# Kernel optimization log

Measured on AMD Instinct MI355X. Metric: run time of the kernel, lower is better.

The kernel has to match this reference:

```python
import jax, jax.numpy as jnp
import numpy as np

# Window-batch of 16x16 windows from a U-Net stage
B, C, H, W = 128, 128, 16, 16
HEADS = 8
EQK, EV = 128, 512      # embed_dim_qk, embed_dim_v (embed_dim=512, ratio=4)
L = H * W               # tokens per window (stride=1)


def _conv3x3(x, w, b):
    # NCHW 3x3 conv, padding 1
    out = jax.lax.conv_general_dilated(x, w, (1, 1), ((1, 1), (1, 1)),
                                       dimension_numbers=('NCHW', 'OIHW', 'NCHW'))
    return out + b[None, :, None, None]


def _pos_att(q, wq, bq, wk, bk, wv, bv, wo, bo, gamma):
    # MultiHeadAttention2D_POS, stride=1 -> conv_q/k/v are 1x1 convs
    hd, hdv = EQK // HEADS, EV // HEADS

    def proj(x, w, bias, d):
        y = jnp.einsum('bchw,ec->behw', x, w) + bias[None, :, None, None]
        return y.reshape(B, HEADS, d, L).transpose(0, 1, 3, 2)  # (B,h,L,d)

    pq = proj(q, wq, bq, hd)
    pk = proj(q, wk, bk, hd)
    pv = proj(q, wv, bv, hdv)
    attn = jax.nn.softmax(jnp.einsum('bhqd,bhkd->bhqk', pq, pk) * hd ** -0.5, axis=-1)
    out = jnp.einsum('bhqk,bhkd->bhqd', attn, pv)
    out = out.transpose(0, 1, 3, 2).reshape(B, EV, H, W)
    out = _conv3x3(out, wo, bo)             # proj_out: 3x3 conv EV->C
    return q + out * gamma                  # gamma-scaled residual


def _cha_att(q, wq, bq, wk, bk, wv, bv, wo, bo, gamma):
    # MultiHeadAttention2D_CHA: depthwise 1x1 grouped convs (channel multiplier = HEADS),
    # attention over the CHANNEL axis. Faithfully reproduces torch's reshape of the
    # group-major (c*HEADS+h) channel layout into (B, heads, C, L).
    def dwproj(x, w, bias):
        y = (x[:, :, None] * w.reshape(C, HEADS)[None, :, :, None, None]
             + bias.reshape(C, HEADS)[None, :, :, None, None])
        return y.reshape(B, C * HEADS, H, W).reshape(B, HEADS, C, L)

    pq = dwproj(q, wq, bq)
    pk = dwproj(q, wk, bk)
    pv = dwproj(q, wv, bv)
    attn = jax.nn.softmax(jnp.einsum('bhcl,bhdl->bhcd', pq, pk) * L ** -0.5, axis=-1)
    out = jnp.einsum('bhcd,bhdl->bhcl', attn, pv)      # (B,h,C,L)
    out = out.reshape(B, HEADS * C, H, W)
    # proj_out: grouped 1x1 ConvTranspose (== grouped 1x1 conv): sum each HEADS-sized group
    out = (out.reshape(B, C, HEADS, H, W)
           * wo.reshape(C, HEADS)[None, :, :, None, None]).sum(2) + bo[None, :, None, None]
    return q + out * gamma


def _forward(qkv_pos, qkv_cha,
             pos_wq, pos_bq, pos_wk, pos_bk, pos_wv, pos_bv, pos_wo, pos_bo, gamma_pos,
             cha_wq, cha_bq, cha_wk, cha_bk, cha_wv, cha_bv, cha_wo, cha_bo, gamma_cha,
             fuse_w, fuse_b):
    out_pos = _pos_att(qkv_pos, pos_wq, pos_bq, pos_wk, pos_bk, pos_wv, pos_bv,
                       pos_wo, pos_bo, gamma_pos)
    out_cha = _cha_att(qkv_cha, cha_wq, cha_bq, cha_wk, cha_bk, cha_wv, cha_bv,
                       cha_wo, cha_bo, gamma_cha)
    out = (out_pos + out_cha) * 0.5          # att_fusion='add' (slides=0 -> full slices)
    return _conv3x3(out, fuse_w, fuse_b)     # conv_out (Dropout2d is identity at eval)


def setup_inputs() -> dict:
    key = jax.random.key(0)
    ks = jax.random.split(key, 24)
    n = lambda k, shape, s=0.05: jax.random.normal(k, shape, dtype=jnp.float32) * s
    return {
        'qkv_pos': jax.random.normal(ks[0], (B, C, H, W), jnp.float32),
        'qkv_cha': jax.random.normal(ks[1], (B, C, H, W), jnp.float32),
        'pos_wq': n(ks[2], (EQK, C)), 'pos_bq': n(ks[3], (EQK,)),
        'pos_wk': n(ks[4], (EQK, C)), 'pos_bk': n(ks[5], (EQK,)),
        'pos_wv': n(ks[6], (EV, C)), 'pos_bv': n(ks[7], (EV,)),
        'pos_wo': n(ks[8], (C, EV, 3, 3)), 'pos_bo': n(ks[9], (C,)),
        'gamma_pos': jnp.array(0.1, jnp.float32),
        'cha_wq': n(ks[10], (C * HEADS,)), 'cha_bq': n(ks[11], (C * HEADS,)),
        'cha_wk': n(ks[12], (C * HEADS,)), 'cha_bk': n(ks[13], (C * HEADS,)),
        'cha_wv': n(ks[14], (C * HEADS,)), 'cha_bv': n(ks[15], (C * HEADS,)),
        'cha_wo': n(ks[16], (C * HEADS,)), 'cha_bo': n(ks[17], (C,)),
        'gamma_cha': jnp.array(0.1, jnp.float32),
        'fuse_w': n(ks[18], (C, C, 3, 3)), 'fuse_b': n(ks[19], (C,)),
    }


def reference(qkv_pos, qkv_cha,
              pos_wq, pos_bq, pos_wk, pos_bk, pos_wv, pos_bv, pos_wo, pos_bo, gamma_pos,
              cha_wq, cha_bq, cha_wk, cha_bk, cha_wv, cha_bv, cha_wo, cha_bo, gamma_cha,
              fuse_w, fuse_b):
    return _forward(qkv_pos, qkv_cha,
                    pos_wq, pos_bq, pos_wk, pos_bk, pos_wv, pos_bv, pos_wo, pos_bo, gamma_pos,
                    cha_wq, cha_bq, cha_wk, cha_bk, cha_wv, cha_bv, cha_wo, cha_bo, gamma_cha,
                    fuse_w, fuse_b)
```

## Files before the change

kernel.cpp:

```cpp
#include <hip/hip_runtime.h>
#include <cstdint>
#include <cstddef>

typedef unsigned short ushort_t;
typedef unsigned int uint_t;
typedef __attribute__((ext_vector_type(8))) short bf16x8;
typedef __attribute__((ext_vector_type(4))) float f32x4;

#define NB 128
#define NC 128
#define NL 256
#define NH 8
#define HD 16
#define HDV 64
#define NEV 512
#define PHALF 4194304

__device__ __forceinline__ ushort_t f2bf(float f) {
    uint_t u = __float_as_uint(f);
    u += 0x7fffu + ((u >> 16) & 1u);
    return (ushort_t)(u >> 16);
}
__device__ __forceinline__ float bf2f(ushort_t s) {
    return __uint_as_float(((uint_t)s) << 16);
}
__device__ __forceinline__ uint_t pack2(float lo, float hi) {
    uint_t r;
    asm("v_cvt_pk_bf16_f32 %0, %1, %2" : "=v"(r) : "v"(lo), "v"(hi));
    return r;
}

template<int CIN>
__global__ __launch_bounds__(256) void k_wpack(const float* __restrict__ w,
                                               short* __restrict__ wp) {
    int idx = blockIdx.x * 256 + threadIdx.x;
    if (idx >= CIN * 1152) return;
    int j    = idx & 7;
    int lane = (idx >> 3) & 63;
    int frag = idx >> 9;
    int rt   = frag & 7;
    int tap  = (frag >> 3) % 9;
    int ch   = frag / 72;
    int co   = rt * 16 + (lane & 15);
    int g    = lane >> 4;
    int ci   = ch * 32 + g * 8 + j;
    wp[idx] = (short)f2bf(w[((size_t)co * CIN + ci) * 9 + tap]);
}

template<int E>
__global__ __launch_bounds__(256) void k_wpack_qkv(const float* __restrict__ w,
                                                   short* __restrict__ wp) {
    int idx = blockIdx.x * 256 + threadIdx.x;
    if (idx >= E * 128) return;
    int j    = idx & 7;
    int lane = (idx >> 3) & 63;
    int ch   = (idx >> 9) & 3;
    int rt   = idx >> 11;
    int n = lane & 15, g = lane >> 4;
    wp[idx] = (short)f2bf(w[(size_t)(rt*16 + n)*128 + ch*32 + g*8 + j]);
}

__global__ __launch_bounds__(256) void k_xpose(const float* __restrict__ x,
                                               ushort_t* __restrict__ xbf) {
    const int half = blockIdx.x, b = blockIdx.y, t = threadIdx.x;
    const float* src = x + (size_t)b*NC*NL + (size_t)half*64*NL + t;
    uint_t* dst = (uint_t*)(xbf + ((size_t)b*NL + t)*NC + half*64);
    #pragma unroll
    for (int k8 = 0; k8 < 8; ++k8) {
        uint4 u;
        u.x = pack2(src[(k8*8+0)*NL], src[(k8*8+1)*NL]);
        u.y = pack2(src[(k8*8+2)*NL], src[(k8*8+3)*NL]);
        u.z = pack2(src[(k8*8+4)*NL], src[(k8*8+5)*NL]);
        u.w = pack2(src[(k8*8+6)*NL], src[(k8*8+7)*NL]);
        *(uint4*)(dst + k8*4) = u;
    }
}

__global__ __launch_bounds__(512, 4) void k_pos_mfma(
    const ushort_t* __restrict__ xbf,
    const short* __restrict__ wpq, const short* __restrict__ wpk,
    const short* __restrict__ wpv,
    const float* __restrict__ bq, const float* __restrict__ bk,
    const float* __restrict__ bv,
    ushort_t* __restrict__ att)
{
    const int h = blockIdx.x, b = blockIdx.y;
    const int t = threadIdx.x;
    const int lane = t & 63, w = t >> 6;
    const int n = lane & 15, g = lane >> 4;

    __shared__ __align__(16) short lds[26112];

    const f32x4 z4 = {0.f, 0.f, 0.f, 0.f};
    f32x4 qacc[2], kacc[2], vacc[4][2];
    #pragma unroll
    for (int ct = 0; ct < 2; ++ct) { qacc[ct] = z4; kacc[ct] = z4; }
    #pragma unroll
    for (int vt = 0; vt < 4; ++vt)
        #pragma unroll
        for (int ct = 0; ct < 2; ++ct) vacc[vt][ct] = z4;

    const ushort_t* xr = xbf + ((size_t)(b*NL + w*32 + n))*NC;

    #pragma unroll 2
    for (int ch = 0; ch < 4; ++ch) {
        bf16x8 xb[2];
        #pragma unroll
        for (int ct = 0; ct < 2; ++ct)
            xb[ct] = *(const bf16x8*)(xr + ct*16*NC + ch*32 + g*8);
        const size_t fo = ((size_t)((h*4 + ch)*64) + lane) * 8;
        {
            bf16x8 aq = *(const bf16x8*)(wpq + fo);
            #pragma unroll
            for (int ct = 0; ct < 2; ++ct)
                qacc[ct] = __builtin_amdgcn_mfma_f32_16x16x32_bf16(aq, xb[ct], qacc[ct], 0, 0, 0);
        }
        {
            bf16x8 ak = *(const bf16x8*)(wpk + fo);
            #pragma unroll
            for (int ct = 0; ct < 2; ++ct)
                kacc[ct] = __builtin_amdgcn_mfma_f32_16x16x32_bf16(ak, xb[ct], kacc[ct], 0, 0, 0);
        }
        #pragma unroll
        for (int vt = 0; vt < 4; ++vt) {
            bf16x8 av = *(const bf16x8*)(wpv + ((size_t)((((h*4 + vt)*4) + ch)*64) + lane) * 8);
            #pragma unroll
            for (int ct = 0; ct < 2; ++ct)
                vacc[vt][ct] = __builtin_amdgcn_mfma_f32_16x16x32_bf16(xb[ct], av, vacc[vt][ct], 0, 0, 0);
        }
    }

    uint_t qu01[2], qu23[2];
    {
        float bqv[4], bkv[4];
        #pragma unroll
        for (int r = 0; r < 4; ++r) {
            bqv[r] = bq[h*16 + g*4 + r];
            bkv[r] = bk[h*16 + g*4 + r];
        }
        #pragma unroll
        for (int ct = 0; ct < 2; ++ct) {
            qu01[ct] = pack2(qacc[ct][0] + bqv[0], qacc[ct][1] + bqv[1]);
            qu23[ct] = pack2(qacc[ct][2] + bqv[2], qacc[ct][3] + bqv[3]);
            uint2 kp;
            kp.x = pack2(kacc[ct][0] + bkv[0], kacc[ct][1] + bkv[1]);
            kp.y = pack2(kacc[ct][2] + bkv[2], kacc[ct][3] + bkv[3]);
            *(uint2*)&lds[(w*32 + ct*16 + n)*16 + g*4] = kp;
        }
        #pragma unroll
        for (int vt = 0; vt < 4; ++vt) {
            const float bvv = bv[h*64 + vt*16 + n];
            #pragma unroll
            for (int ct = 0; ct < 2; ++ct) {
                uint2 vp;
                vp.x = pack2(vacc[vt][ct][0] + bvv, vacc[vt][ct][1] + bvv);
                vp.y = pack2(vacc[vt][ct][2] + bvv, vacc[vt][ct][3] + bvv);
                *(uint2*)&lds[9216 + (vt*16 + n)*264 + w*32 + ct*16 + g*4] = vp;
            }
        }
    }
    __syncthreads();

    const int a0 = (n + 32*(g & 1)) * 4;
    #pragma unroll 1
    for (int qt = 0; qt < 2; ++qt) {
        union { uint_t u[4]; bf16x8 v; } qfu;
        qfu.u[0] = (uint_t)__builtin_amdgcn_ds_bpermute(a0,      (int)qu01[qt]);
        qfu.u[1] = (uint_t)__builtin_amdgcn_ds_bpermute(a0,      (int)qu23[qt]);
        qfu.u[2] = (uint_t)__builtin_amdgcn_ds_bpermute(a0 + 64, (int)qu01[qt]);
        qfu.u[3] = (uint_t)__builtin_amdgcn_ds_bpermute(a0 + 64, (int)qu23[qt]);
        if (g >= 2) { qfu.u[0] = 0; qfu.u[1] = 0; qfu.u[2] = 0; qfu.u[3] = 0; }
        bf16x8 qf = qfu.v;

        f32x4 s[16];
        #pragma unroll
        for (int kt = 0; kt < 16; ++kt) {
            bf16x8 kf = (bf16x8){0,0,0,0,0,0,0,0};
            if (g < 2) kf = *(const bf16x8*)&lds[(kt*16 + n)*16 + g*8];
            s[kt] = __builtin_amdgcn_mfma_f32_16x16x32_bf16(kf, qf, z4, 0, 0, 0);
        }
        float d0 = 0.f, d1 = 0.f, d2 = 0.f, d3 = 0.f;
        #pragma unroll
        for (int kt = 0; kt < 16; ++kt) {
            float e0 = exp2f(s[kt][0] * 0.36067376022224085f);
            float e1 = exp2f(s[kt][1] * 0.36067376022224085f);
            float e2 = exp2f(s[kt][2] * 0.36067376022224085f);
            float e3 = exp2f(s[kt][3] * 0.36067376022224085f);
            s[kt][0] = e0; s[kt][1] = e1; s[kt][2] = e2; s[kt][3] = e3;
            d0 += e0; d1 += e1; d2 += e2; d3 += e3;
        }
        float den = (d0 + d1) + (d2 + d3);
        den += __shfl_xor(den, 16);
        den += __shfl_xor(den, 32);
        const float inv = 1.f / den;

        f32x4 oacc[4] = {z4, z4, z4, z4};
        #pragma unroll
        for (int c2 = 0; c2 < 8; ++c2) {
            #pragma unroll
            for (int u = 0; u < 2; ++u) {
                const int kt = 2*c2 + u;
                uint2 pp;
                pp.x = pack2(s[kt][0], s[kt][1]);
                pp.y = pack2(s[kt][2], s[kt][3]);
                *(uint2*)&lds[4096 + w*640 + n*40 + u*16 + g*4] = pp;
            }
            bf16x8 pf = *(const bf16x8*)&lds[4096 + w*640 + n*40 + g*8];
            #pragma unroll
            for (int vt = 0; vt < 4; ++vt) {
                bf16x8 av = *(const bf16x8*)&lds[9216 + (vt*16 + n)*264 + c2*32 + g*8];
                oacc[vt] = __builtin_amdgcn_mfma_f32_16x16x32_bf16(av, pf, oacc[vt], 0, 0, 0);
            }
        }
        ushort_t* ap = att + (((size_t)b*NL + (w*32 + qt*16 + n))*NEV + h*HDV + g*4);
        #pragma unroll
        for (int vt = 0; vt < 4; ++vt) {
            uint2 op;
            op.x = pack2(oacc[vt][0]*inv, oacc[vt][1]*inv);
            op.y = pack2(oacc[vt][2]*inv, oacc[vt][3]*inv);
            *(uint2*)(ap + vt*16) = op;
        }
    }
}

__global__ __launch_bounds__(256, 2) void k_conv_ci(
    const ushort_t* __restrict__ att, const short* __restrict__ wp,
    ushort_t* __restrict__ P)
{
    const int kc = blockIdx.x >> 1, lh = blockIdx.x & 1, b = blockIdx.y;
    const int t = threadIdx.x;
    const int lane = t & 63, w = t >> 6;
    const int wr = w >> 1, wc = w & 1;
    const int n = lane & 15, gl = lane >> 4;
    const int y0 = lh * 8;

    __shared__ __align__(16) short ims[2][5760];

    {
        bf16x8 z = {0,0,0,0,0,0,0,0};
        bf16x8* p = (bf16x8*)&ims[0][0];
        for (int i = t; i < 1440; i += 256) p[i] = z;
    }

    f32x4 acc[4][4];
    #pragma unroll
    for (int i = 0; i < 4; ++i)
        #pragma unroll
        for (int j = 0; j < 4; ++j) acc[i][j] = (f32x4){0.f,0.f,0.f,0.f};

    const int gg1 = t & 3,        xx1 = (t >> 2) & 15,        yp1 = t >> 6;
    const int id2 = t + 256;
    const int gg2 = id2 & 3,      xx2 = (id2 >> 2) & 15,      yp2 = id2 >> 6;
    const int id3 = t + 512;
    const int gg3 = id3 & 3,      xx3 = (id3 >> 2) & 15,      yp3 = id3 >> 6;
    const bool has3 = (t < 128);
    const int y1 = y0 - 1 + yp1, y2 = y0 - 1 + yp2, y3 = y0 - 1 + yp3;
    const bool ok1 = (y1 >= 0) && (y1 < 16);
    const bool ok2 = (y2 >= 0) && (y2 < 16);
    const bool ok3 = has3 && (y3 >= 0) && (y3 < 16);
    const ushort_t* src1 = att + ((size_t)(b*NL + y1*16 + xx1))*NEV + kc*256 + gg1*8;
    const ushort_t* src2 = att + ((size_t)(b*NL + y2*16 + xx2))*NEV + kc*256 + gg2*8;
    const ushort_t* src3 = att + ((size_t)(b*NL + y3*16 + xx3))*NEV + kc*256 + gg3*8;
    const int slot1 = ((yp1*4 + gg1)*18 + xx1 + 1) * 8;
    const int slot2 = ((yp2*4 + gg2)*18 + xx2 + 1) * 8;
    const int slot3 = ((yp3*4 + gg3)*18 + xx3 + 1) * 8;

    bf16x8 v1 = {0,0,0,0,0,0,0,0}, v2 = v1, v3 = v1;
    if (ok1) v1 = *(const bf16x8*)src1;
    if (ok2) v2 = *(const bf16x8*)src2;
    if (ok3) v3 = *(const bf16x8*)src3;

    const short* wpl = wp + (size_t)lane * 8;
    bf16x8 Ac[4], An[4], Bc[4], Bn[4];
    #pragma unroll
    for (int i = 0; i < 4; ++i) { An[i] = (bf16x8){0,0,0,0,0,0,0,0}; Bn[i] = An[i]; Bc[i] = An[i]; }
    #pragma unroll
    for (int rt = 0; rt < 4; ++rt)
        Ac[rt] = *(const bf16x8*)(wpl + ((size_t)((kc*8*9)*8 + wr*4 + rt)) * 512);

    __syncthreads();

    #pragma unroll 1
    for (int ch = 0; ch < 8; ++ch) {
        short* buf = &ims[ch & 1][0];
        *(bf16x8*)&buf[slot1] = v1;
        *(bf16x8*)&buf[slot2] = v2;
        if (has3) *(bf16x8*)&buf[slot3] = v3;
        if (ch < 7) {
            if (ok1) v1 = *(const bf16x8*)(src1 + (ch + 1) * 32);
            if (ok2) v2 = *(const bf16x8*)(src2 + (ch + 1) * 32);
            if (ok3) v3 = *(const bf16x8*)(src3 + (ch + 1) * 32);
        }
        __syncthreads();
        #pragma unroll
        for (int ct = 0; ct < 4; ++ct)
            Bc[ct] = *(const bf16x8*)&buf[(((wc*4 + ct)*4 + gl)*18 + n) * 8];
        #pragma unroll
        for (int tap = 0; tap < 9; ++tap) {
            if (tap < 8) {
                const int dy = (tap + 1) / 3, dx = (tap + 1) % 3;
                #pragma unroll
                for (int rt = 0; rt < 4; ++rt)
                    An[rt] = *(const bf16x8*)(wpl +
                        ((size_t)(((kc*8 + ch)*9 + tap + 1)*8 + wr*4 + rt)) * 512);
                #pragma unroll
                for (int ct = 0; ct < 4; ++ct)
                    Bn[ct] = *(const bf16x8*)&buf[(((wc*4 + ct + dy)*4 + gl)*18 + n + dx) * 8];
            } else if (ch < 7) {
                #pragma unroll
                for (int rt = 0; rt < 4; ++rt)
                    An[rt] = *(const bf16x8*)(wpl +
                        ((size_t)(((kc*8 + ch + 1)*9)*8 + wr*4 + rt)) * 512);
            }
            #pragma unroll
            for (int rt = 0; rt < 4; ++rt)
                #pragma unroll
                for (int ct = 0; ct < 4; ++ct)
                    acc[rt][ct] = __builtin_amdgcn_mfma_f32_16x16x32_bf16(
                        Ac[rt], Bc[ct], acc[rt][ct], 0, 0, 0);
            #pragma unroll
            for (int i = 0; i < 4; ++i) {
                if (tap < 8 || ch < 7) Ac[i] = An[i];
                if (tap < 8)           Bc[i] = Bn[i];
            }
        }
    }

    ushort_t* Pb = P + (size_t)kc * PHALF + (size_t)b * NL * NC;
    #pragma unroll
    for (int rt = 0; rt < 4; ++rt) {
        const int co0 = wr*64 + rt*16 + gl*4;
        #pragma unroll
        for (int ct = 0; ct < 4; ++ct) {
            const int l = lh*128 + wc*64 + ct*16 + n;
            uint2 u;
            u.x = pack2(acc[rt][ct][0], acc[rt][ct][1]);
            u.y = pack2(acc[rt][ct][2], acc[rt][ct][3]);
            *(uint2*)(Pb + (size_t)l*NC + co0) = u;
        }
    }
}

__global__ __launch_bounds__(256, 2) void k_conv_co(
    const float* __restrict__ comb, const short* __restrict__ wp,
    const float* __restrict__ bias, float* __restrict__ out)
{
    const int kc = blockIdx.x >> 1, lh = blockIdx.x & 1, b = blockIdx.y;
    const int t = threadIdx.x;
    const int lane = t & 63, w = t >> 6;
    const int wr = w >> 1, wc = w & 1;
    const int n = lane & 15, gl = lane >> 4;
    const int y0 = lh * 8;

    __shared__ __align__(16) short ims[2][5760];

    {
        bf16x8 z = {0,0,0,0,0,0,0,0};
        bf16x8* p = (bf16x8*)&ims[0][0];
        for (int i = t; i < 1440; i += 256) p[i] = z;
    }

    f32x4 acc[2][4];
    #pragma unroll
    for (int i = 0; i < 2; ++i)
        #pragma unroll
        for (int j = 0; j < 4; ++j) acc[i][j] = (f32x4){0.f,0.f,0.f,0.f};

    const int gg1 = t & 3,        xx1 = (t >> 2) & 15,        yp1 = t >> 6;
    const int id2 = t + 256;
    const int gg2 = id2 & 3,      xx2 = (id2 >> 2) & 15,      yp2 = id2 >> 6;
    const int id3 = t + 512;
    const int gg3 = id3 & 3,      xx3 = (id3 >> 2) & 15,      yp3 = id3 >> 6;
    const bool has3 = (t < 128);
    const int y1 = y0 - 1 + yp1, y2 = y0 - 1 + yp2, y3 = y0 - 1 + yp3;
    const bool ok1 = (y1 >= 0) && (y1 < 16);
    const bool ok2 = (y2 >= 0) && (y2 < 16);
    const bool ok3 = has3 && (y3 >= 0) && (y3 < 16);
    const float* s1 = comb + ((size_t)(b*NL + y1*16 + xx1))*NC + gg1*8;
    const float* s2 = comb + ((size_t)(b*NL + y2*16 + xx2))*NC + gg2*8;
    const float* s3 = comb + ((size_t)(b*NL + y3*16 + xx3))*NC + gg3*8;
    const int slot1 = ((yp1*4 + gg1)*18 + xx1 + 1) * 8;
    const int slot2 = ((yp2*4 + gg2)*18 + xx2 + 1) * 8;
    const int slot3 = ((yp3*4 + gg3)*18 + xx3 + 1) * 8;

    float4 f1a, f1b, f2a, f2b, f3a, f3b;
    f1a = f1b = f2a = f2b = f3a = f3b = (float4){0.f,0.f,0.f,0.f};
    if (ok1) { f1a = *(const float4*)s1; f1b = *(const float4*)(s1 + 4); }
    if (ok2) { f2a = *(const float4*)s2; f2b = *(const float4*)(s2 + 4); }
    if (ok3) { f3a = *(const float4*)s3; f3b = *(const float4*)(s3 + 4); }

    const short* wpl = wp + (size_t)lane * 8;
    bf16x8 Ac[2], An[2], Bc[4], Bn[4];
    #pragma unroll
    for (int i = 0; i < 2; ++i) An[i] = (bf16x8){0,0,0,0,0,0,0,0};
    #pragma unroll
    for (int i = 0; i < 4; ++i) { Bn[i] = (bf16x8){0,0,0,0,0,0,0,0}; Bc[i] = Bn[i]; }
    #pragma unroll
    for (int rt = 0; rt < 2; ++rt)
        Ac[rt] = *(const bf16x8*)(wpl + ((size_t)(kc*4 + wr*2 + rt)) * 512);

    __syncthreads();

    #pragma unroll 1
    for (int ch = 0; ch < 4; ++ch) {
        short* buf = &ims[ch & 1][0];
        uint4 w1, w2, w3;
        w1.x = pack2(f1a.x, f1a.y);  w1.y = pack2(f1a.z, f1a.w);
        w1.z = pack2(f1b.x, f1b.y);  w1.w = pack2(f1b.z, f1b.w);
        w2.x = pack2(f2a.x, f2a.y);  w2.y = pack2(f2a.z, f2a.w);
        w2.z = pack2(f2b.x, f2b.y);  w2.w = pack2(f2b.z, f2b.w);
        w3.x = pack2(f3a.x, f3a.y);  w3.y = pack2(f3a.z, f3a.w);
        w3.z = pack2(f3b.x, f3b.y);  w3.w = pack2(f3b.z, f3b.w);
        *(uint4*)&buf[slot1] = w1;
        *(uint4*)&buf[slot2] = w2;
        if (has3) *(uint4*)&buf[slot3] = w3;
        if (ch < 3) {
            if (ok1) { f1a = *(const float4*)(s1 + (ch+1)*32); f1b = *(const float4*)(s1 + (ch+1)*32 + 4); }
            if (ok2) { f2a = *(const float4*)(s2 + (ch+1)*32); f2b = *(const float4*)(s2 + (ch+1)*32 + 4); }
            if (ok3) { f3a = *(const float4*)(s3 + (ch+1)*32); f3b = *(const float4*)(s3 + (ch+1)*32 + 4); }
        }
        __syncthreads();
        #pragma unroll
        for (int ct = 0; ct < 4; ++ct)
            Bc[ct] = *(const bf16x8*)&buf[(((wc*4 + ct)*4 + gl)*18 + n) * 8];
        #pragma unroll
        for (int tap = 0; tap < 9; ++tap) {
            if (tap < 8) {
                const int dy = (tap + 1) / 3, dx = (tap + 1) % 3;
                #pragma unroll
                for (int rt = 0; rt < 2; ++rt)
                    An[rt] = *(const bf16x8*)(wpl +
                        ((size_t)((ch*9 + tap + 1)*8 + kc*4 + wr*2 + rt)) * 512);
                #pragma unroll
                for (int ct = 0; ct < 4; ++ct)
                    Bn[ct] = *(const bf16x8*)&buf[(((wc*4 + ct + dy)*4 + gl)*18 + n + dx) * 8];
            } else if (ch < 3) {
                #pragma unroll
                for (int rt = 0; rt < 2; ++rt)
                    An[rt] = *(const bf16x8*)(wpl +
                        ((size_t)((ch + 1)*9*8 + kc*4 + wr*2 + rt)) * 512);
            }
            #pragma unroll
            for (int rt = 0; rt < 2; ++rt)
                #pragma unroll
                for (int ct = 0; ct < 4; ++ct)
                    acc[rt][ct] = __builtin_amdgcn_mfma_f32_16x16x32_bf16(
                        Ac[rt], Bc[ct], acc[rt][ct], 0, 0, 0);
            #pragma unroll
            for (int i = 0; i < 2; ++i)
                if (tap < 8 || ch < 3) Ac[i] = An[i];
            #pragma unroll
            for (int i = 0; i < 4; ++i)
                if (tap < 8) Bc[i] = Bn[i];
        }
    }

    #pragma unroll
    for (int rt = 0; rt < 2; ++rt) {
        const int co0 = kc*64 + wr*32 + rt*16 + gl*4;
        const float c0 = bias[co0+0], c1 = bias[co0+1],
                    c2 = bias[co0+2], c3 = bias[co0+3];
        #pragma unroll
        for (int ct = 0; ct < 4; ++ct) {
            const int l = lh*128 + wc*64 + ct*16 + n;
            f32x4 a = acc[rt][ct];
            out[((size_t)b*NC + co0+0)*NL + l] = c0 + a[0];
            out[((size_t)b*NC + co0+1)*NL + l] = c1 + a[1];
            out[((size_t)b*NC + co0+2)*NL + l] = c2 + a[2];
            out[((size_t)b*NC + co0+3)*NL + l] = c3 + a[3];
        }
    }
}

#define NLP 260
__global__ __launch_bounds__(256) void k_cha(
    const float* __restrict__ xc,
    const float* __restrict__ cwq, const float* __restrict__ cbq,
    const float* __restrict__ cwk, const float* __restrict__ cbk,
    const float* __restrict__ cwv, const float* __restrict__ cbv,
    const float* __restrict__ cwo, const float* __restrict__ cbo,
    const float* __restrict__ gamma,
    const ushort_t* __restrict__ P, const float* __restrict__ qpos,
    const float* __restrict__ pbo, const float* __restrict__ gpos,
    float* __restrict__ comb)
{
    const int h = blockIdx.x, b = blockIdx.y, t = threadIdx.x;
    __shared__ float qh[16][NLP];
    __shared__ float G_s[16][17];
    __shared__ float S_s[16];
    __shared__ float wq_s[128], bq_s[128], wk_s[128], bk_s[128], wv_s[128], bv_s[128];
    __shared__ float A_s[128][17];
    __shared__ float B_s[128];
    __shared__ float M_s[16][17];
    __shared__ float c_s[16];

    #pragma unroll
    for (int j = 0; j < 16; ++j)
        qh[j][t] = xc[((size_t)b*NC + h*16 + j)*NL + t];
    if (t < 128) {
        const int k = h*128 + t;
        wq_s[t] = cwq[k]; bq_s[t] = cbq[k];
        wk_s[t] = cwk[k]; bk_s[t] = cbk[k];
        wv_s[t] = cwv[k]; bv_s[t] = cbv[k];
    }
    __syncthreads();
    {
        const int i = t >> 4, j = t & 15;
        const float4* qi = (const float4*)qh[i];
        const float4* qj = (const float4*)qh[j];
        float gg = 0.f;
        for (int l4 = 0; l4 < NL/4; ++l4) {
            float4 a = qi[l4], c = qj[l4];
            gg = fmaf(a.x,c.x,fmaf(a.y,c.y,fmaf(a.z,c.z,fmaf(a.w,c.w,gg))));
        }
        G_s[i][j] = gg;
    }
    if (t < 16) {
        const float4* qi = (const float4*)qh[t];
        float s = 0.f;
        for (int l4 = 0; l4 < NL/4; ++l4) { float4 a = qi[l4]; s += a.x + a.y + a.z + a.w; }
        S_s[t] = s;
    }
    __syncthreads();
    if (t < 128) {
        const int c2 = t, cg = c2 >> 3;
        const float wqc = wq_s[c2], bqc = bq_s[c2];
        float Pv[16];
        #pragma unroll
        for (int j = 0; j < 16; ++j) Pv[j] = wqc*G_s[cg][j] + bqc*S_s[j];
        const float Qc = wqc*S_s[cg] + bqc*256.0f;
        float mx = -3.0e38f;
        #pragma unroll
        for (int dg = 0; dg < 16; ++dg) {
            #pragma unroll
            for (int dj = 0; dj < 8; ++dj) {
                const int d = dg*8 + dj;
                float s = wk_s[d]*Pv[dg] + bk_s[d]*Qc;
                mx = fmaxf(mx, s);
            }
        }
        float A[16];
        #pragma unroll
        for (int j = 0; j < 16; ++j) A[j] = 0.f;
        float Bv = 0.f, den = 0.f;
        #pragma unroll
        for (int dg = 0; dg < 16; ++dg) {
            #pragma unroll
            for (int dj = 0; dj < 8; ++dj) {
                const int d = dg*8 + dj;
                float s = wk_s[d]*Pv[dg] + bk_s[d]*Qc;
                float e = __expf((s - mx) * 0.0625f);
                den += e;
                A[dg] = fmaf(e, wv_s[d], A[dg]);
                Bv = fmaf(e, bv_s[d], Bv);
            }
        }
        const float inv = 1.f / den;
        #pragma unroll
        for (int j = 0; j < 16; ++j) A_s[c2][j] = A[j]*inv;
        B_s[c2] = Bv*inv;
    }
    __syncthreads();
    {
        const int cl = t >> 4, j = t & 15;
        const int cp = h*16 + cl;
        float m = 0.f;
        #pragma unroll
        for (int hp = 0; hp < 8; ++hp)
            m = fmaf(cwo[cp*8+hp], A_s[cl*8+hp][j], m);
        M_s[cl][j] = m;
        if (j == 0) {
            float cc = cbo[cp];
            #pragma unroll
            for (int hp = 0; hp < 8; ++hp)
                cc = fmaf(cwo[cp*8+hp], B_s[cl*8+hp], cc);
            c_s[cl] = cc;
        }
    }
    __syncthreads();
    {
        const float g  = gamma[0];
        const float gp = gpos[0];
        const int l = t;
        float av[16];
        #pragma unroll
        for (int cl = 0; cl < 16; ++cl) {
            float a = c_s[cl];
            #pragma unroll
            for (int j = 0; j < 16; ++j)
                a = fmaf(M_s[cl][j], qh[j][l], a);
            av[cl] = a;
        }
        const ushort_t* p0 = P + ((size_t)b*NL + l)*NC + h*16;
        const ushort_t* p1 = p0 + PHALF;
        const float* qp = qpos + ((size_t)b*NC + h*16)*NL + l;
        float4* cp4 = (float4*)(comb + ((size_t)b*NL + l)*NC + h*16);
        #pragma unroll
        for (int q = 0; q < 4; ++q) {
            uint2 u0 = *(const uint2*)(p0 + 4*q);
            uint2 u1 = *(const uint2*)(p1 + 4*q);
            float s0 = bf2f((ushort_t)(u0.x & 0xffffu)) + bf2f((ushort_t)(u1.x & 0xffffu));
            float s1 = bf2f((ushort_t)(u0.x >> 16))     + bf2f((ushort_t)(u1.x >> 16));
            float s2 = bf2f((ushort_t)(u0.y & 0xffffu)) + bf2f((ushort_t)(u1.y & 0xffffu));
            float s3 = bf2f((ushort_t)(u0.y >> 16))     + bf2f((ushort_t)(u1.y >> 16));
            float4 c;
            c.x = 0.5f*(qp[(4*q+0)*NL] + gp*(pbo[h*16+4*q+0] + s0) + qh[4*q+0][l] + g*av[4*q+0]);
            c.y = 0.5f*(qp[(4*q+1)*NL] + gp*(pbo[h*16+4*q+1] + s1) + qh[4*q+1][l] + g*av[4*q+1]);
            c.z = 0.5f*(qp[(4*q+2)*NL] + gp*(pbo[h*16+4*q+2] + s2) + qh[4*q+2][l] + g*av[4*q+2]);
            c.w = 0.5f*(qp[(4*q+3)*NL] + gp*(pbo[h*16+4*q+3] + s3) + qh[4*q+3][l] + g*av[4*q+3]);
            cp4[q] = c;
        }
    }
}

extern "C" void kernel_launch(void* const* d_in, const int* in_sizes, int n_in,
                              void* d_out, int out_size, void* d_ws, size_t ws_size,
                              hipStream_t stream)
{
    const float* qpos = (const float*)d_in[0];
    const float* qcha = (const float*)d_in[1];
    const float* pwq  = (const float*)d_in[2];
    const float* pbq  = (const float*)d_in[3];
    const float* pwk  = (const float*)d_in[4];
    const float* pbk  = (const float*)d_in[5];
    const float* pwv  = (const float*)d_in[6];
    const float* pbv  = (const float*)d_in[7];
    const float* pwo  = (const float*)d_in[8];
    const float* pbo  = (const float*)d_in[9];
    const float* gpos = (const float*)d_in[10];
    const float* cwq  = (const float*)d_in[11];
    const float* cbq  = (const float*)d_in[12];
    const float* cwk  = (const float*)d_in[13];
    const float* cbk  = (const float*)d_in[14];
    const float* cwv  = (const float*)d_in[15];
    const float* cbv  = (const float*)d_in[16];
    const float* cwo  = (const float*)d_in[17];
    const float* cbo  = (const float*)d_in[18];
    const float* gcha = (const float*)d_in[19];
    const float* fw   = (const float*)d_in[20];
    const float* fb   = (const float*)d_in[21];
    float* outp = (float*)d_out;

    char* ws = (char*)d_ws;
    ushort_t* att  = (ushort_t*)ws;
    float*    comb = (float*)ws;
    ushort_t* P    = (ushort_t*)(ws + 33554432);
    ushort_t* xbf  = (ushort_t*)(ws + 33554432);
    short*    wp1  = (short*)(ws + 50331648);
    short*    wp2  = (short*)(ws + 51511296);
    short*    wpq  = (short*)(ws + 51806208);
    short*    wpk  = (short*)(ws + 51838976);
    short*    wpv  = (short*)(ws + 51871744);

    k_wpack<NEV><<<dim3((NEV*1152 + 255)/256), 256, 0, stream>>>(pwo, wp1);
    k_wpack<NC ><<<dim3((NC *1152 + 255)/256), 256, 0, stream>>>(fw,  wp2);
    k_wpack_qkv<128><<<dim3(64),  256, 0, stream>>>(pwq, wpq);
    k_wpack_qkv<128><<<dim3(64),  256, 0, stream>>>(pwk, wpk);
    k_wpack_qkv<512><<<dim3(256), 256, 0, stream>>>(pwv, wpv);

    k_xpose<<<dim3(2, NB), 256, 0, stream>>>(qpos, xbf);
    k_pos_mfma<<<dim3(NH, NB), 512, 0, stream>>>(xbf, wpq, wpk, wpv,
                                                 pbq, pbk, pbv, att);
    k_conv_ci<<<dim3(4, NB), 256, 0, stream>>>(att, wp1, P);
    k_cha<<<dim3(NH, NB), 256, 0, stream>>>(qcha, cwq, cbq, cwk, cbk, cwv, cbv,
                                            cwo, cbo, gcha,
                                            P, qpos, pbo, gpos, comb);
    k_conv_co<<<dim3(4, NB), 256, 0, stream>>>(comb, wp2, fb, outp);
}
```

Measured before the change: 172.1 us.

## Interleave packed conv weights per lane and triple-buffer weight fragment prefetch

```diff
diff --git a/kernel.cpp b/kernel.cpp
--- a/kernel.cpp
+++ b/kernel.cpp
@@ -30,20 +30,21 @@
     return r;
 }
 
-template<int CIN>
+template<int CIN, int GRP>
 __global__ __launch_bounds__(256) void k_wpack(const float* __restrict__ w,
                                                short* __restrict__ wp) {
     int idx = blockIdx.x * 256 + threadIdx.x;
     if (idx >= CIN * 1152) return;
+    constexpr int LG = (GRP == 4) ? 2 : 1;
     int j    = idx & 7;
-    int lane = (idx >> 3) & 63;
-    int frag = idx >> 9;
-    int rt   = frag & 7;
-    int tap  = (frag >> 3) % 9;
-    int ch   = frag / 72;
-    int co   = rt * 16 + (lane & 15);
-    int g    = lane >> 4;
-    int ci   = ch * 32 + g * 8 + j;
+    int r    = (idx >> 3) & (GRP - 1);
+    int lane = (idx >> (3 + LG)) & 63;
+    int gidx = (idx >> (9 + LG)) & ((8 / GRP) - 1);
+    int tc   = idx >> 12;
+    int tap  = tc % 9;
+    int ch   = tc / 9;
+    int co   = (gidx * GRP + r) * 16 + (lane & 15);
+    int ci   = ch * 32 + (lane >> 4) * 8 + j;
     wp[idx] = (short)f2bf(w[((size_t)co * CIN + ci) * 9 + tap]);
 }
 
@@ -270,59 +271,63 @@
     if (ok2) v2 = *(const bf16x8*)src2;
     if (ok3) v3 = *(const bf16x8*)src3;
 
-    const short* wpl = wp + (size_t)lane * 8;
-    bf16x8 Ac[4], An[4], Bc[4], Bn[4];
-    #pragma unroll
-    for (int i = 0; i < 4; ++i) { An[i] = (bf16x8){0,0,0,0,0,0,0,0}; Bn[i] = An[i]; Bc[i] = An[i]; }
-    #pragma unroll
-    for (int rt = 0; rt < 4; ++rt)
-        Ac[rt] = *(const bf16x8*)(wpl + ((size_t)((kc*8*9)*8 + wr*4 + rt)) * 512);
+    const short* wpl = wp + (size_t)lane * 32;
+    auto Aaddr = [&](int ch16, int tap) {
+        return (const bf16x8*)(wpl + ((size_t)((ch16*9 + tap)*2 + wr)) * 2048);
+    };
+
+    bf16x8 Abuf[3][4];
+    bf16x8 Bc[4], Bn[4];
+    #pragma unroll
+    for (int i = 0; i < 4; ++i) { Bc[i] = (bf16x8){0,0,0,0,0,0,0,0}; Bn[i] = Bc[i]; }
 
     __syncthreads();
 
     #pragma unroll 1
     for (int ch = 0; ch < 8; ++ch) {
+        const int ch16 = kc*8 + ch;
         short* buf = &ims[ch & 1][0];
         *(bf16x8*)&buf[slot1] = v1;
         *(bf16x8*)&buf[slot2] = v2;
         if (has3) *(bf16x8*)&buf[slot3] = v3;
+        __syncthreads();
         if (ch < 7) {
             if (ok1) v1 = *(const bf16x8*)(src1 + (ch + 1) * 32);
             if (ok2) v2 = *(const bf16x8*)(src2 + (ch + 1) * 32);
             if (ok3) v3 = *(const bf16x8*)(src3 + (ch + 1) * 32);
         }
-        __syncthreads();
+        #pragma unroll
+        for (int p = 0; p < 3; ++p) {
+            const bf16x8* ap = Aaddr(ch16, p);
+            #pragma unroll
+            for (int rt = 0; rt < 4; ++rt) Abuf[p][rt] = ap[rt];
+        }
         #pragma unroll
         for (int ct = 0; ct < 4; ++ct)
             Bc[ct] = *(const bf16x8*)&buf[(((wc*4 + ct)*4 + gl)*18 + n) * 8];
+
         #pragma unroll
         for (int tap = 0; tap < 9; ++tap) {
             if (tap < 8) {
                 const int dy = (tap + 1) / 3, dx = (tap + 1) % 3;
                 #pragma unroll
-                for (int rt = 0; rt < 4; ++rt)
-                    An[rt] = *(const bf16x8*)(wpl +
-                        ((size_t)(((kc*8 + ch)*9 + tap + 1)*8 + wr*4 + rt)) * 512);
-                #pragma unroll
                 for (int ct = 0; ct < 4; ++ct)
                     Bn[ct] = *(const bf16x8*)&buf[(((wc*4 + ct + dy)*4 + gl)*18 + n + dx) * 8];
-            } else if (ch < 7) {
-                #pragma unroll
-                for (int rt = 0; rt < 4; ++rt)
-                    An[rt] = *(const bf16x8*)(wpl +
-                        ((size_t)(((kc*8 + ch + 1)*9)*8 + wr*4 + rt)) * 512);
             }
             #pragma unroll
             for (int rt = 0; rt < 4; ++rt)
                 #pragma unroll
                 for (int ct = 0; ct < 4; ++ct)
                     acc[rt][ct] = __builtin_amdgcn_mfma_f32_16x16x32_bf16(
-                        Ac[rt], Bc[ct], acc[rt][ct], 0, 0, 0);
-            #pragma unroll
-            for (int i = 0; i < 4; ++i) {
-                if (tap < 8 || ch < 7) Ac[i] = An[i];
-                if (tap < 8)           Bc[i] = Bn[i];
-            }
+                        Abuf[tap % 3][rt], Bc[ct], acc[rt][ct], 0, 0, 0);
+            if (tap + 3 < 9) {
+                const bf16x8* ap = Aaddr(ch16, tap + 3);
+                #pragma unroll
+                for (int rt = 0; rt < 4; ++rt) Abuf[tap % 3][rt] = ap[rt];
+            }
+            #pragma unroll
+            for (int i = 0; i < 4; ++i)
+                if (tap < 8) Bc[i] = Bn[i];
         }
     }
 
@@ -389,15 +394,15 @@
     if (ok2) { f2a = *(const float4*)s2; f2b = *(const float4*)(s2 + 4); }
     if (ok3) { f3a = *(const float4*)s3; f3b = *(const float4*)(s3 + 4); }
 
-    const short* wpl = wp + (size_t)lane * 8;
-    bf16x8 Ac[2], An[2], Bc[4], Bn[4];
-    #pragma unroll
-    for (int i = 0; i < 2; ++i) An[i] = (bf16x8){0,0,0,0,0,0,0,0};
-    #pragma unroll
-    for (int i = 0; i < 4; ++i) { Bn[i] = (bf16x8){0,0,0,0,0,0,0,0}; Bc[i] = Bn[i]; }
-    #pragma unroll
-    for (int rt = 0; rt < 2; ++rt)
-        Ac[rt] = *(const bf16x8*)(wpl + ((size_t)(kc*4 + wr*2 + rt)) * 512);
+    const short* wpl = wp + (size_t)lane * 16;
+    auto Aaddr = [&](int ch, int tap) {
+        return (const bf16x8*)(wpl + ((size_t)((ch*9 + tap)*4 + kc*2 + wr)) * 1024);
+    };
+
+    bf16x8 Abuf[3][2];
+    bf16x8 Bc[4], Bn[4];
+    #pragma unroll
+    for (int i = 0; i < 4; ++i) { Bc[i] = (bf16x8){0,0,0,0,0,0,0,0}; Bn[i] = Bc[i]; }
 
     __syncthreads();
 
@@ -414,41 +419,41 @@
         *(uint4*)&buf[slot1] = w1;
         *(uint4*)&buf[slot2] = w2;
         if (has3) *(uint4*)&buf[slot3] = w3;
+        __syncthreads();
         if (ch < 3) {
             if (ok1) { f1a = *(const float4*)(s1 + (ch+1)*32); f1b = *(const float4*)(s1 + (ch+1)*32 + 4); }
             if (ok2) { f2a = *(const float4*)(s2 + (ch+1)*32); f2b = *(const float4*)(s2 + (ch+1)*32 + 4); }
             if (ok3) { f3a = *(const float4*)(s3 + (ch+1)*32); f3b = *(const float4*)(s3 + (ch+1)*32 + 4); }
         }
-        __syncthreads();
+        #pragma unroll
+        for (int p = 0; p < 3; ++p) {
+            const bf16x8* ap = Aaddr(ch, p);
+            #pragma unroll
+            for (int rt = 0; rt < 2; ++rt) Abuf[p][rt] = ap[rt];
+        }
         #pragma unroll
         for (int ct = 0; ct < 4; ++ct)
             Bc[ct] = *(const bf16x8*)&buf[(((wc*4 + ct)*4 + gl)*18 + n) * 8];
+
         #pragma unroll
         for (int tap = 0; tap < 9; ++tap) {
             if (tap < 8) {
                 const int dy = (tap + 1) / 3, dx = (tap + 1) % 3;
                 #pragma unroll
-                for (int rt = 0; rt < 2; ++rt)
-                    An[rt] = *(const bf16x8*)(wpl +
-                        ((size_t)((ch*9 + tap + 1)*8 + kc*4 + wr*2 + rt)) * 512);
-                #pragma unroll
                 for (int ct = 0; ct < 4; ++ct)
                     Bn[ct] = *(const bf16x8*)&buf[(((wc*4 + ct + dy)*4 + gl)*18 + n + dx) * 8];
-            } else if (ch < 3) {
-                #pragma unroll
-                for (int rt = 0; rt < 2; ++rt)
-                    An[rt] = *(const bf16x8*)(wpl +
-                        ((size_t)((ch + 1)*9*8 + kc*4 + wr*2 + rt)) * 512);
             }
             #pragma unroll
             for (int rt = 0; rt < 2; ++rt)
                 #pragma unroll
                 for (int ct = 0; ct < 4; ++ct)
                     acc[rt][ct] = __builtin_amdgcn_mfma_f32_16x16x32_bf16(
-                        Ac[rt], Bc[ct], acc[rt][ct], 0, 0, 0);
-            #pragma unroll
-            for (int i = 0; i < 2; ++i)
-                if (tap < 8 || ch < 3) Ac[i] = An[i];
+                        Abuf[tap % 3][rt], Bc[ct], acc[rt][ct], 0, 0, 0);
+            if (tap + 3 < 9) {
+                const bf16x8* ap = Aaddr(ch, tap + 3);
+                #pragma unroll
+                for (int rt = 0; rt < 2; ++rt) Abuf[tap % 3][rt] = ap[rt];
+            }
             #pragma unroll
             for (int i = 0; i < 4; ++i)
                 if (tap < 8) Bc[i] = Bn[i];
@@ -652,8 +657,8 @@
     short*    wpk  = (short*)(ws + 51838976);
     short*    wpv  = (short*)(ws + 51871744);
 
-    k_wpack<NEV><<<dim3((NEV*1152 + 255)/256), 256, 0, stream>>>(pwo, wp1);
-    k_wpack<NC ><<<dim3((NC *1152 + 255)/256), 256, 0, stream>>>(fw,  wp2);
+    k_wpack<NEV, 4><<<dim3((NEV*1152 + 255)/256), 256, 0, stream>>>(pwo, wp1);
+    k_wpack<NC,  2><<<dim3((NC *1152 + 255)/256), 256, 0, stream>>>(fw,  wp2);
     k_wpack_qkv<128><<<dim3(64),  256, 0, stream>>>(pwq, wpq);
     k_wpack_qkv<128><<<dim3(64),  256, 0, stream>>>(pwk, wpk);
     k_wpack_qkv<512><<<dim3(256), 256, 0, stream>>>(pwv, wpv);
```

After: 170.1 us. Within noise of the previous version (-1.2%).
